# Kernel optimization log

Hardware: AMD Instinct MI355X
Metric: run time of the kernel (lower is better)

Reference implementation:

```python
import jax, jax.numpy as jnp
import numpy as np

P_SIZE = 128   # proto_size
HID = 768      # hidden_size
BATCH = 32
NREL = 16
RATIO = 0.5    # proto_emb_ratio


def setup_inputs() -> dict:
    key = jax.random.key(0)
    k1, k2, k3, k4 = jax.random.split(key, 4)
    return {
        "instance_embedding": jax.random.normal(k1, (BATCH, HID), jnp.float32),
        # small scale keeps sigmoid(p_h @ M_r @ p_t) away from hard saturation
        "relation_embedding": jax.random.normal(k2, (NREL, HID, HID), jnp.float32) * 0.02,
        "rel_label_ids": jax.random.randint(k3, (BATCH, NREL, P_SIZE), 0, P_SIZE + 1, dtype=jnp.int32),
        "labels": jnp.arange(BATCH, dtype=jnp.int32),  # distinct -> torch.unique is exact with static shapes
        "prototypes": jax.random.normal(k4, (P_SIZE, HID), jnp.float32),  # nn.Embedding weight
    }


def reference(instance_embedding, relation_embedding, rel_label_ids, labels, prototypes):
    P, H = prototypes.shape
    B, R, _ = rel_label_ids.shape

    # torch.unique(labels, return_inverse=True): sorted uniques + inverse map.
    labels_unique = jnp.sort(labels)                      # [K] (K == B, labels distinct)
    inv = jnp.argsort(jnp.argsort(labels))                # index_list (rank of each label)
    # original code: index = index_list[k] -> rel rows permuted by inverse map
    rel_k = rel_label_ids[inv]                            # [K,R,P]

    total_nonzero = jnp.sum(rel_label_ids) > 0
    batch_mask = (jnp.sum(rel_k, axis=(1, 2)) > 0)[:, None, None]   # skip if sum(rel[index])==0
    row_mask = (jnp.sum(rel_k, axis=2) > 0)[:, :, None]             # skip if sum(rel[index][i])==0
    m = (rel_k != P) & batch_mask & row_mask & total_nonzero        # [K,R,P] active entries
    mf = m.astype(prototypes.dtype)

    P0 = prototypes                                       # get_proto_embedding(): never updated inside loop
    heads = jnp.minimum(rel_k, P - 1)                     # safe gather (masked where == P)
    Ph = P0[heads]                                        # [K,R,P,H]  (largest intermediate)
    pt = P0[labels_unique]                                # [K,H]

    # sim[k,i,j] = sigmoid(P0[head] @ M_r[i] @ P0[label_k])
    v = jnp.einsum('rhg,kg->krh', relation_embedding, pt)           # [K,R,H]
    sim = jax.nn.sigmoid(jnp.einsum('krph,krh->krp', Ph, v))        # [K,R,P]

    # logits_ol init: zeros, then logits_ol[:][:][:][0] = 1.0 sets the k==0 slab to 1.0
    base = jnp.zeros((B, R, P, 2), prototypes.dtype).at[0].set(1.0)
    l1 = jnp.where(m, sim, base[..., 1])
    l0 = jnp.where(m, 1.0 - sim, base[..., 0])
    logits_ol = jnp.stack([l0, l1], axis=-1).reshape(-1, 2)         # [K*R*P, 2]
    labels_ol = m.astype(jnp.int32).reshape(-1)                     # [K*R*P]

    # proto propagation: mean over active (i,j) of P0[head] @ M_r[i]
    w = jnp.einsum('krp,krph->krh', mf, Ph)                         # [K,R,H]
    prop = jnp.einsum('krh,rhg->kg', w, relation_embedding)         # [K,H]
    n = jnp.sum(mf, axis=(1, 2))                                    # num_prop per k
    prop = prop / jnp.maximum(n, 1.0)[:, None]
    old_rows = prototypes[labels_unique]
    new_rows = RATIO * old_rows + (1.0 - RATIO) * prop
    rows = jnp.where((n > 0)[:, None], new_rows, old_rows)
    proto_embedding = prototypes.at[labels_unique].set(rows)        # scatter update (distinct rows)

    # CrossEntropyLoss (mean); 0 when all rel ids are zero (labels_ol would be None)
    logp = jax.nn.log_softmax(logits_ol, axis=-1)
    ce = -jnp.mean(jnp.take_along_axis(logp, labels_ol[:, None], axis=1))
    loss_ol = jnp.where(total_nonzero, ce, 0.0)

    # logits = -||proto - instance||^2 pairwise: [B, P]
    diff = instance_embedding[:, None, :] - proto_embedding[None, :, :]
    logits = -jnp.sum(diff * diff, axis=2)

    return logits, loss_ol, proto_embedding
```

## Files before the change

kernel.cpp:

```cpp
#include <hip/hip_runtime.h>
#include <hip/hip_bf16.h>
#include <math.h>

#define K_B 32
#define NRELD 16
#define PSZ 128
#define HID 768

using bf16x8 = __attribute__((ext_vector_type(8))) short;
using f32x4  = __attribute__((ext_vector_type(4))) float;

__device__ __forceinline__ unsigned int f2bf(float x) {
    unsigned int u = __float_as_uint(x);
    return (u + 0x7fffu + ((u >> 16) & 1u)) >> 16;
}
__device__ __forceinline__ float bf2f(unsigned short b) {
    return __uint_as_float(((unsigned int)b) << 16);
}

__global__ __launch_bounds__(512) void k_setup(const int* __restrict__ labels,
        const int* __restrict__ rel, int* __restrict__ inv, int* __restrict__ lu,
        int* __restrict__ rowflag, int* __restrict__ batchflag,
        int* __restrict__ total, int* __restrict__ rowOwner,
        float* __restrict__ nAct, float* __restrict__ lossAcc,
        float* __restrict__ prop)
{
    __shared__ int lab[32], rankS[32], luS[32], ownS[128];
    __shared__ int rowflagS[512], cntS[512], bfS[32], totS;
    int t = threadIdx.x;
    if (t < 32) lab[t] = labels[t];
    __syncthreads();
    if (t < 32) {
        int r = 0;
        for (int j = 0; j < 32; ++j) r += (lab[j] < lab[t]);
        rankS[t] = r; inv[t] = r;
    }
    if (t < 128) ownS[t] = -1;
    __syncthreads();
    if (t < 32) luS[rankS[t]] = lab[t];
    __syncthreads();
    if (t < 32) { lu[t] = luS[t]; ownS[luS[t]] = t; }
    __syncthreads();
    if (t < 128) rowOwner[t] = ownS[t];
    {
        int k = t >> 4, i = t & 15;
        const int* rp = rel + ((size_t)rankS[k] * NRELD + i) * PSZ;
        int s = 0, c = 0;
        for (int j = 0; j < PSZ; ++j) { int v_ = rp[j]; s += v_; c += (v_ != PSZ); }
        rowflagS[t] = (s > 0); cntS[t] = c;
        rowflag[t] = (s > 0);
    }
    __syncthreads();
    if (t < 32) {
        int b = 0;
        for (int i = 0; i < 16; ++i) b |= rowflagS[t*16 + i];
        bfS[t] = b; batchflag[t] = b;
    }
    __syncthreads();
    if (t == 0) {
        int tt = 0;
        for (int k = 0; k < 32; ++k) tt |= bfS[k];
        totS = tt; total[0] = tt; lossAcc[0] = 0.f;
    }
    __syncthreads();
    if (t < 32) {
        float n = 0.f;
        if (totS && bfS[t])
            for (int i = 0; i < 16; ++i)
                if (rowflagS[t*16 + i]) n += (float)cntS[t*16 + i];
        nAct[t] = n;
    }
    for (int idx = t; idx < K_B*HID; idx += 512) prop[idx] = 0.f;
}

__global__ __launch_bounds__(192) void k_prep(
        const int* __restrict__ relIds, const int* __restrict__ inv,
        const int* __restrict__ rowflag, const int* __restrict__ batchflag,
        const int* __restrict__ total, const int* __restrict__ rowOwner,
        const float* __restrict__ P0,
        unsigned short* __restrict__ S_bf, unsigned short* __restrict__ P0_bf,
        unsigned short* __restrict__ P0T_bf, unsigned short* __restrict__ pt_bf)
{
    int bid = blockIdx.x, t = threadIdx.x;
    int k = bid >> 4, r = bid & 15;
    __shared__ int hist[128];
    if (t < 128) hist[t] = 0;
    __syncthreads();
    int flag = total[0] && batchflag[k] && rowflag[k*NRELD + r];
    if (flag && t < 128) {
        int id = relIds[((size_t)inv[k]*NRELD + r)*PSZ + t];
        if (id != PSZ) atomicAdd(&hist[id], 1);
    }
    __syncthreads();
    if (t < 128) S_bf[(size_t)bid*128 + t] = (unsigned short)f2bf((float)hist[t]);
    if (bid < 128) {
        int p = bid;
        float4 v4 = *(const float4*)&P0[(size_t)p*HID + t*4];
        unsigned int b0 = f2bf(v4.x), b1 = f2bf(v4.y), b2 = f2bf(v4.z), b3 = f2bf(v4.w);
        uint2 d; d.x = b0 | (b1 << 16); d.y = b2 | (b3 << 16);
        *(uint2*)&P0_bf[(size_t)p*HID + t*4] = d;
        P0T_bf[(size_t)(t*4+0)*128 + p] = (unsigned short)b0;
        P0T_bf[(size_t)(t*4+1)*128 + p] = (unsigned short)b1;
        P0T_bf[(size_t)(t*4+2)*128 + p] = (unsigned short)b2;
        P0T_bf[(size_t)(t*4+3)*128 + p] = (unsigned short)b3;
        int kk = rowOwner[p];
        if (kk >= 0) *(uint2*)&pt_bf[(size_t)kk*HID + t*4] = d;
    }
}

__global__ __launch_bounds__(256) void k_v_mfma(
        const float* __restrict__ rel, const unsigned short* __restrict__ pt_bf,
        unsigned short* __restrict__ v_bf)
{
    int r = blockIdx.x, hs = blockIdx.y, t = threadIdx.x;
    int wave = t >> 6, lane = t & 63;
    __shared__ unsigned short ptS[32*768];
    __shared__ unsigned short AS[64*128];

    for (int i = t; i < 3072; i += 256) {
        int k = i / 96, c = i % 96;
        uint4 d = *(const uint4*)&pt_bf[(size_t)k*HID + c*8];
        *(uint4*)&ptS[k*768 + (c ^ (k & 7))*8] = d;
    }

    const int gq = (t & 31) * 4;
    const int hr = t >> 5;
    const size_t relbase = ((size_t)r*HID + hs*64) * HID;

    float4 buf[8];
    #pragma unroll
    for (int rr = 0; rr < 8; ++rr)
        buf[rr] = *(const float4*)&rel[relbase + (size_t)(hr + rr*8)*HID + gq];

    f32x4 acc[2] = {{0.f,0.f,0.f,0.f},{0.f,0.f,0.f,0.f}};
    const int arow = wave*16 + (lane & 15);

    for (int gt = 0; gt < 6; ++gt) {
        int g0 = gt * 128;
        __syncthreads();
        #pragma unroll
        for (int rr = 0; rr < 8; ++rr) {
            int h_l = hr + rr*8;
            float4 v4 = buf[rr];
            int cs = (gq >> 3) ^ (h_l & 7);
            uint2 d; d.x = f2bf(v4.x) | (f2bf(v4.y) << 16);
            d.y = f2bf(v4.z) | (f2bf(v4.w) << 16);
            *(uint2*)&AS[h_l*128 + cs*8 + (gq & 4)] = d;
        }
        __syncthreads();
        if (gt < 5) {
            int gn = g0 + 128;
            #pragma unroll
            for (int rr = 0; rr < 8; ++rr)
                buf[rr] = *(const float4*)&rel[relbase + (size_t)(hr + rr*8)*HID + gn + gq];
        }
        #pragma unroll
        for (int kk = 0; kk < 4; ++kk) {
            int cA = (kk*4 + (lane >> 4)) ^ (arow & 7);
            bf16x8 a = *(const bf16x8*)&AS[arow*128 + cA*8];
            #pragma unroll
            for (int nf = 0; nf < 2; ++nf) {
                int k = nf*16 + (lane & 15);
                int cB = (gt*16 + kk*4 + (lane >> 4)) ^ (k & 7);
                bf16x8 b = *(const bf16x8*)&ptS[k*768 + cB*8];
                acc[nf] = __builtin_amdgcn_mfma_f32_16x16x32_bf16(a, b, acc[nf], 0, 0, 0);
            }
        }
    }
    int h_out = hs*64 + wave*16 + (lane >> 4) * 4;
    #pragma unroll
    for (int nf = 0; nf < 2; ++nf) {
        int k = nf*16 + (lane & 15);
        uint2 d; d.x = f2bf(acc[nf][0]) | (f2bf(acc[nf][1]) << 16);
        d.y = f2bf(acc[nf][2]) | (f2bf(acc[nf][3]) << 16);
        *(uint2*)&v_bf[((size_t)k*NRELD + r)*HID + h_out] = d;
    }
}

__global__ __launch_bounds__(256) void k_w_mfma(
        const unsigned short* __restrict__ S_bf, const unsigned short* __restrict__ P0T_bf,
        unsigned short* __restrict__ w_bf)
{
    int ms = blockIdx.x, ns = blockIdx.y, t = threadIdx.x;
    int wave = t >> 6, lane = t & 63;
    __shared__ unsigned short AS[64*128], BS2[64*128];
    for (int i = t; i < 1024; i += 256) {
        int row = i >> 4, c = i & 15;
        *(uint4*)&AS[row*128 + (c ^ (row & 7))*8] =
            *(const uint4*)&S_bf[(size_t)(ms*64 + row)*128 + c*8];
        *(uint4*)&BS2[row*128 + (c ^ (row & 7))*8] =
            *(const uint4*)&P0T_bf[(size_t)(ns*64 + row)*128 + c*8];
    }
    __syncthreads();
    f32x4 acc[4] = {{0.f,0.f,0.f,0.f},{0.f,0.f,0.f,0.f},{0.f,0.f,0.f,0.f},{0.f,0.f,0.f,0.f}};
    int arow = wave*16 + (lane & 15);
    #pragma unroll
    for (int kk = 0; kk < 4; ++kk) {
        int cA = (kk*4 + (lane >> 4)) ^ (arow & 7);
        bf16x8 a = *(const bf16x8*)&AS[arow*128 + cA*8];
        #pragma unroll
        for (int nf = 0; nf < 4; ++nf) {
            int brow = nf*16 + (lane & 15);
            int cB = (kk*4 + (lane >> 4)) ^ (brow & 7);
            bf16x8 b = *(const bf16x8*)&BS2[brow*128 + cB*8];
            acc[nf] = __builtin_amdgcn_mfma_f32_16x16x32_bf16(a, b, acc[nf], 0, 0, 0);
        }
    }
    int kr0 = ms*64 + wave*16 + (lane >> 4) * 4;
    #pragma unroll
    for (int nf = 0; nf < 4; ++nf) {
        int h = ns*64 + nf*16 + (lane & 15);
        #pragma unroll
        for (int j = 0; j < 4; ++j)
            w_bf[(size_t)(kr0 + j)*HID + h] = (unsigned short)f2bf(acc[nf][j]);
    }
}

__global__ __launch_bounds__(256) void k_prop_mfma(
        const float* __restrict__ rel, const unsigned short* __restrict__ w_bf,
        float* __restrict__ prop)
{
    int r = blockIdx.x, gs = blockIdx.y, t = threadIdx.x;
    int wave = t >> 6, lane = t & 63;
    __shared__ unsigned short WS[32*768];
    __shared__ unsigned short BS[64*128];

    for (int i = t; i < 3072; i += 256) {
        int k = i / 96, c = i % 96;
        uint4 d = *(const uint4*)&w_bf[((size_t)k*NRELD + r)*HID + c*8];
        *(uint4*)&WS[k*768 + (c ^ (k & 7))*8] = d;
    }

    const int gqq = t & 15;
    const int h4  = t >> 4;
    const size_t relb = (size_t)r*HID*HID + (size_t)gs*64;

    float4 buf[8];
    #pragma unroll
    for (int sup = 0; sup < 2; ++sup)
        #pragma unroll
        for (int rr = 0; rr < 4; ++rr)
            buf[sup*4+rr] = *(const float4*)&rel[relb + (size_t)(sup*64 + h4*4 + rr)*HID + gqq*4];

    f32x4 acc[2] = {{0.f,0.f,0.f,0.f},{0.f,0.f,0.f,0.f}};

    for (int ht = 0; ht < 6; ++ht) {
        int ht0 = ht * 128;
        __syncthreads();
        #pragma unroll
        for (int sup = 0; sup < 2; ++sup) {
            #pragma unroll
            for (int i = 0; i < 4; ++i) {
                int g_l = gqq*4 + i;
                int hloc = sup*64 + h4*4;
                unsigned int p0 = f2bf(((const float*)&buf[sup*4+0])[i]);
                unsigned int p1 = f2bf(((const float*)&buf[sup*4+1])[i]);
                unsigned int p2 = f2bf(((const float*)&buf[sup*4+2])[i]);
                unsigned int p3 = f2bf(((const float*)&buf[sup*4+3])[i]);
                int cs = (hloc >> 3) ^ ((g_l >> 2) & 7);
                uint2 d; d.x = p0 | (p1 << 16); d.y = p2 | (p3 << 16);
                *(uint2*)&BS[g_l*128 + cs*8 + (hloc & 4)] = d;
            }
        }
        __syncthreads();
        if (ht < 5) {
            int hn = ht0 + 128;
            #pragma unroll
            for (int sup = 0; sup < 2; ++sup)
                #pragma unroll
                for (int rr = 0; rr < 4; ++rr)
                    buf[sup*4+rr] = *(const float4*)&rel[relb + (size_t)(hn + sup*64 + h4*4 + rr)*HID + gqq*4];
        }
        int g_l = wave*16 + (lane & 15);
        #pragma unroll
        for (int kk = 0; kk < 4; ++kk) {
            int cB = (kk*4 + (lane >> 4)) ^ ((g_l >> 2) & 7);
            bf16x8 b = *(const bf16x8*)&BS[g_l*128 + cB*8];
            #pragma unroll
            for (int mf = 0; mf < 2; ++mf) {
                int arow = mf*16 + (lane & 15);
                int cA = (ht*16 + kk*4 + (lane >> 4)) ^ (arow & 7);
                bf16x8 a = *(const bf16x8*)&WS[arow*768 + cA*8];
                acc[mf] = __builtin_amdgcn_mfma_f32_16x16x32_bf16(a, b, acc[mf], 0, 0, 0);
            }
        }
    }
    int gcol = gs*64 + wave*16 + (lane & 15);
    #pragma unroll
    for (int mf = 0; mf < 2; ++mf) {
        int k0 = mf*16 + (lane >> 4) * 4;
        #pragma unroll
        for (int j = 0; j < 4; ++j)
            atomicAdd(&prop[(size_t)(k0 + j)*HID + gcol], acc[mf][j]);
    }
}

__global__ __launch_bounds__(256) void k_zzloss(
        const unsigned short* __restrict__ v_bf, const unsigned short* __restrict__ P0_bf,
        const unsigned short* __restrict__ S_bf, float* __restrict__ lossAcc)
{
    int ms = blockIdx.x, t = threadIdx.x;
    int wave = t >> 6, lane = t & 63;
    __shared__ unsigned short AS[16*128], BS2[128*128];
    __shared__ float red[256];
    f32x4 acc[2] = {{0.f,0.f,0.f,0.f},{0.f,0.f,0.f,0.f}};

    for (int ht = 0; ht < 6; ++ht) {
        int h0 = ht * 128;
        __syncthreads();
        {
            int row = t >> 4, c = t & 15;
            *(uint4*)&AS[row*128 + (c ^ (row & 7))*8] =
                *(const uint4*)&v_bf[(size_t)(ms*16 + row)*HID + h0 + c*8];
            #pragma unroll
            for (int q = 0; q < 8; ++q) {
                int j2 = t + q*256;
                int prow = j2 >> 4, c2 = j2 & 15;
                *(uint4*)&BS2[prow*128 + (c2 ^ (prow & 7))*8] =
                    *(const uint4*)&P0_bf[(size_t)prow*HID + h0 + c2*8];
            }
        }
        __syncthreads();
        int arow = lane & 15;
        #pragma unroll
        for (int kk = 0; kk < 4; ++kk) {
            int cA = (kk*4 + (lane >> 4)) ^ (arow & 7);
            bf16x8 a = *(const bf16x8*)&AS[arow*128 + cA*8];
            #pragma unroll
            for (int nf = 0; nf < 2; ++nf) {
                int brow = wave*32 + nf*16 + (lane & 15);
                int cB = (kk*4 + (lane >> 4)) ^ (brow & 7);
                bf16x8 b = *(const bf16x8*)&BS2[brow*128 + cB*8];
                acc[nf] = __builtin_amdgcn_mfma_f32_16x16x32_bf16(a, b, acc[nf], 0, 0, 0);
            }
        }
    }
    float term = 0.f;
    #pragma unroll
    for (int nf = 0; nf < 2; ++nf) {
        int p = wave*32 + nf*16 + (lane & 15);
        int kr0 = ms*16 + (lane >> 4) * 4;
        #pragma unroll
        for (int j = 0; j < 4; ++j) {
            float S = bf2f(S_bf[(size_t)(kr0 + j)*128 + p]);
            if (S != 0.f) {
                float z = acc[nf][j];
                float s = 1.f / (1.f + expf(-z));
                term += S * (logf(expf(1.f - s) + expf(s)) - s);
            }
        }
    }
    red[t] = term;
    __syncthreads();
    for (int off = 128; off; off >>= 1) {
        if (t < off) red[t] += red[t + off];
        __syncthreads();
    }
    if (t == 0) atomicAdd(lossAcc, red[0]);
}

__global__ __launch_bounds__(192) void k_proto(const float* __restrict__ P0,
        const float* __restrict__ prop, const float* __restrict__ nAct,
        const int* __restrict__ rowOwner, float* __restrict__ protoOut)
{
    int p = blockIdx.x, t = threadIdx.x;
    float4 old = *(const float4*)&P0[(size_t)p*HID + t*4];
    float4 o = old;
    int k = rowOwner[p];
    if (k >= 0) {
        float n = nAct[k];
        if (n > 0.f) {
            float4 pr = *(const float4*)&prop[(size_t)k*HID + t*4];
            float invn = 1.f/n;
            o.x = 0.5f*old.x + 0.5f*pr.x*invn;
            o.y = 0.5f*old.y + 0.5f*pr.y*invn;
            o.z = 0.5f*old.z + 0.5f*pr.z*invn;
            o.w = 0.5f*old.w + 0.5f*pr.w*invn;
        }
    }
    *(float4*)&protoOut[(size_t)p*HID + t*4] = o;
}

__global__ __launch_bounds__(128) void k_logits(const float* __restrict__ inst,
        const float* __restrict__ protoOut, const float* __restrict__ lossAcc,
        const int* __restrict__ total, const float* __restrict__ nAct,
        float* __restrict__ outLogits, float* __restrict__ outLoss)
{
    int b = blockIdx.x, t = threadIdx.x;
    __shared__ float iS[768];
    for (int q = 0; q < 6; ++q) iS[t + 128*q] = inst[(size_t)b*HID + t + 128*q];
    __syncthreads();
    const float4* pr = (const float4*)&protoOut[(size_t)t*HID];
    float acc = 0.f;
    for (int q = 0; q < HID/4; ++q) {
        float4 pv = pr[q];
        float dx = iS[q*4+0] - pv.x, dy = iS[q*4+1] - pv.y;
        float dz = iS[q*4+2] - pv.z, dw = iS[q*4+3] - pv.w;
        acc += dx*dx + dy*dy + dz*dz + dw*dw;
    }
    outLogits[b*PSZ + t] = -acc;
    if (b == 0 && t == 0) {
        float na = 0.f;
        for (int k = 0; k < 32; ++k) na += nAct[k];
        outLoss[0] = total[0]
            ? (lossAcc[0] + (65536.f - na) * 0.6931471805599453f) * (1.f/65536.f)
            : 0.f;
    }
}

extern "C" void kernel_launch(void* const* d_in, const int* in_sizes, int n_in,
                              void* d_out, int out_size, void* d_ws, size_t ws_size,
                              hipStream_t stream)
{
    const float* inst  = (const float*)d_in[0];
    const float* rel   = (const float*)d_in[1];
    const int* relIds  = (const int*)d_in[2];
    const int* labels  = (const int*)d_in[3];
    const float* P0    = (const float*)d_in[4];
    float* out = (float*)d_out;
    float* outLogits = out;
    float* outLoss   = out + 4096;
    float* outProto  = out + 4097;

    char* ws = (char*)d_ws;
    unsigned short* v_bf    = (unsigned short*)(ws + 0);
    unsigned short* w_bf    = (unsigned short*)(ws + 786432);
    unsigned short* S_bf    = (unsigned short*)(ws + 1572864);
    unsigned short* P0_bf   = (unsigned short*)(ws + 1703936);
    unsigned short* P0T_bf  = (unsigned short*)(ws + 1900544);
    unsigned short* pt_bf   = (unsigned short*)(ws + 2097152);
    float* prop    = (float*)(ws + 2146304);
    float* nAct    = (float*)(ws + 2244608);
    float* lossAcc = (float*)(ws + 2244736);
    int*   inv     = (int*)(ws + 2244864);
    int*   lu      = (int*)(ws + 2244992);
    int*   rowflag = (int*)(ws + 2245120);
    int*   batchflag = (int*)(ws + 2247168);
    int*   total   = (int*)(ws + 2247296);
    int*   rowOwner= (int*)(ws + 2247424);

    k_setup<<<1, 512, 0, stream>>>(labels, relIds, inv, lu, rowflag, batchflag,
                                   total, rowOwner, nAct, lossAcc, prop);
    k_prep<<<512, 192, 0, stream>>>(relIds, inv, rowflag, batchflag, total,
                                    rowOwner, P0, S_bf, P0_bf, P0T_bf, pt_bf);
    k_v_mfma<<<dim3(16,12), 256, 0, stream>>>(rel, pt_bf, v_bf);
    k_w_mfma<<<dim3(8,12), 256, 0, stream>>>(S_bf, P0T_bf, w_bf);
    k_prop_mfma<<<dim3(16,12), 256, 0, stream>>>(rel, w_bf, prop);
    k_zzloss<<<32, 256, 0, stream>>>(v_bf, P0_bf, S_bf, lossAcc);
    k_proto<<<128, 192, 0, stream>>>(P0, prop, nAct, rowOwner, outProto);
    k_logits<<<32, 128, 0, stream>>>(inst, outProto, lossAcc, total, nAct,
                                     outLogits, outLoss);
}
```

Baseline: 150.7 us.

## Fuse setup into prep, merge v/w GEMMs and loss/proto kernels

Drops the single-block setup kernel. Each prep block now recomputes label ranks and owners in shared memory and derives its own row flag and active count with a block reduction. The v and w MFMA kernels are merged into one 288-block launch that also zeroes prop and the loss accumulator. The loss and proto-update kernels are merged into one launch, with the proto blocks rebuilding per-row active counts from the per-row flags. The aim is to cut launch count from eight to five and remove the serial single-block setup stage, at the cost of redundant rank computation in every prep block and uneven work across blocks in the merged kernels.

```diff
diff --git a/kernel.cpp b/kernel.cpp
--- a/kernel.cpp
+++ b/kernel.cpp
@@ -18,81 +18,48 @@
     return __uint_as_float(((unsigned int)b) << 16);
 }
 
-__global__ __launch_bounds__(512) void k_setup(const int* __restrict__ labels,
-        const int* __restrict__ rel, int* __restrict__ inv, int* __restrict__ lu,
-        int* __restrict__ rowflag, int* __restrict__ batchflag,
-        int* __restrict__ total, int* __restrict__ rowOwner,
-        float* __restrict__ nAct, float* __restrict__ lossAcc,
-        float* __restrict__ prop)
-{
-    __shared__ int lab[32], rankS[32], luS[32], ownS[128];
-    __shared__ int rowflagS[512], cntS[512], bfS[32], totS;
-    int t = threadIdx.x;
-    if (t < 32) lab[t] = labels[t];
-    __syncthreads();
-    if (t < 32) {
-        int r = 0;
-        for (int j = 0; j < 32; ++j) r += (lab[j] < lab[t]);
-        rankS[t] = r; inv[t] = r;
-    }
-    if (t < 128) ownS[t] = -1;
-    __syncthreads();
-    if (t < 32) luS[rankS[t]] = lab[t];
-    __syncthreads();
-    if (t < 32) { lu[t] = luS[t]; ownS[luS[t]] = t; }
-    __syncthreads();
-    if (t < 128) rowOwner[t] = ownS[t];
-    {
-        int k = t >> 4, i = t & 15;
-        const int* rp = rel + ((size_t)rankS[k] * NRELD + i) * PSZ;
-        int s = 0, c = 0;
-        for (int j = 0; j < PSZ; ++j) { int v_ = rp[j]; s += v_; c += (v_ != PSZ); }
-        rowflagS[t] = (s > 0); cntS[t] = c;
-        rowflag[t] = (s > 0);
-    }
-    __syncthreads();
-    if (t < 32) {
-        int b = 0;
-        for (int i = 0; i < 16; ++i) b |= rowflagS[t*16 + i];
-        bfS[t] = b; batchflag[t] = b;
-    }
-    __syncthreads();
-    if (t == 0) {
-        int tt = 0;
-        for (int k = 0; k < 32; ++k) tt |= bfS[k];
-        totS = tt; total[0] = tt; lossAcc[0] = 0.f;
-    }
-    __syncthreads();
-    if (t < 32) {
-        float n = 0.f;
-        if (totS && bfS[t])
-            for (int i = 0; i < 16; ++i)
-                if (rowflagS[t*16 + i]) n += (float)cntS[t*16 + i];
-        nAct[t] = n;
-    }
-    for (int idx = t; idx < K_B*HID; idx += 512) prop[idx] = 0.f;
-}
-
 __global__ __launch_bounds__(192) void k_prep(
-        const int* __restrict__ relIds, const int* __restrict__ inv,
-        const int* __restrict__ rowflag, const int* __restrict__ batchflag,
-        const int* __restrict__ total, const int* __restrict__ rowOwner,
+        const int* __restrict__ labels, const int* __restrict__ relIds,
         const float* __restrict__ P0,
         unsigned short* __restrict__ S_bf, unsigned short* __restrict__ P0_bf,
-        unsigned short* __restrict__ P0T_bf, unsigned short* __restrict__ pt_bf)
+        unsigned short* __restrict__ P0T_bf, unsigned short* __restrict__ pt_bf,
+        int* __restrict__ rowflag, int* __restrict__ cntRow,
+        int* __restrict__ rowOwner_g)
 {
     int bid = blockIdx.x, t = threadIdx.x;
     int k = bid >> 4, r = bid & 15;
-    __shared__ int hist[128];
-    if (t < 128) hist[t] = 0;
-    __syncthreads();
-    int flag = total[0] && batchflag[k] && rowflag[k*NRELD + r];
-    if (flag && t < 128) {
-        int id = relIds[((size_t)inv[k]*NRELD + r)*PSZ + t];
-        if (id != PSZ) atomicAdd(&hist[id], 1);
-    }
-    __syncthreads();
-    if (t < 128) S_bf[(size_t)bid*128 + t] = (unsigned short)f2bf((float)hist[t]);
+    __shared__ int lab[32], rankS[32], luS[32], ownS[128];
+    __shared__ int hist[128], redS[128];
+    if (t < 32) lab[t] = labels[t];
+    if (t < 128) { hist[t] = 0; ownS[t] = -1; }
+    __syncthreads();
+    if (t < 32) { int rk = 0; for (int j = 0; j < 32; ++j) rk += (lab[j] < lab[t]); rankS[t] = rk; }
+    __syncthreads();
+    if (t < 32) luS[rankS[t]] = lab[t];
+    __syncthreads();
+    if (t < 32) ownS[luS[t]] = t;
+    __syncthreads();
+
+    int id = 0, isv = 0;
+    if (t < 128) {
+        id = relIds[((size_t)rankS[k]*NRELD + r)*PSZ + t];
+        isv = (id != PSZ);
+        if (isv) atomicAdd(&hist[id], 1);
+        redS[t] = id + (isv << 20);
+    }
+    __syncthreads();
+    for (int off = 64; off; off >>= 1) {
+        if (t < off) redS[t] += redS[t + off];
+        __syncthreads();
+    }
+    int rowsum = redS[0] & 0xFFFFF;
+    int cnt    = redS[0] >> 20;
+    int rf     = (rowsum > 0);
+    if (t < 128)
+        S_bf[(size_t)bid*128 + t] = (unsigned short)f2bf(rf ? (float)hist[t] : 0.f);
+    if (t == 0) { rowflag[bid] = rf; cntRow[bid] = cnt; }
+    if (bid == 0 && t < 128) rowOwner_g[t] = ownS[t];
+
     if (bid < 128) {
         int p = bid;
         float4 v4 = *(const float4*)&P0[(size_t)p*HID + t*4];
@@ -103,116 +70,120 @@
         P0T_bf[(size_t)(t*4+1)*128 + p] = (unsigned short)b1;
         P0T_bf[(size_t)(t*4+2)*128 + p] = (unsigned short)b2;
         P0T_bf[(size_t)(t*4+3)*128 + p] = (unsigned short)b3;
-        int kk = rowOwner[p];
+        int kk = ownS[p];
         if (kk >= 0) *(uint2*)&pt_bf[(size_t)kk*HID + t*4] = d;
     }
 }
 
-__global__ __launch_bounds__(256) void k_v_mfma(
+__global__ __launch_bounds__(256) void k_vw(
         const float* __restrict__ rel, const unsigned short* __restrict__ pt_bf,
-        unsigned short* __restrict__ v_bf)
-{
-    int r = blockIdx.x, hs = blockIdx.y, t = threadIdx.x;
+        const unsigned short* __restrict__ S_bf, const unsigned short* __restrict__ P0T_bf,
+        unsigned short* __restrict__ v_bf, unsigned short* __restrict__ w_bf,
+        float* __restrict__ prop, float* __restrict__ lossAcc)
+{
+    __shared__ unsigned short sh[32*768 + 64*128];
+    int bid = blockIdx.x, t = threadIdx.x;
     int wave = t >> 6, lane = t & 63;
-    __shared__ unsigned short ptS[32*768];
-    __shared__ unsigned short AS[64*128];
-
-    for (int i = t; i < 3072; i += 256) {
-        int k = i / 96, c = i % 96;
-        uint4 d = *(const uint4*)&pt_bf[(size_t)k*HID + c*8];
-        *(uint4*)&ptS[k*768 + (c ^ (k & 7))*8] = d;
-    }
-
-    const int gq = (t & 31) * 4;
-    const int hr = t >> 5;
-    const size_t relbase = ((size_t)r*HID + hs*64) * HID;
-
-    float4 buf[8];
-    #pragma unroll
-    for (int rr = 0; rr < 8; ++rr)
-        buf[rr] = *(const float4*)&rel[relbase + (size_t)(hr + rr*8)*HID + gq];
-
-    f32x4 acc[2] = {{0.f,0.f,0.f,0.f},{0.f,0.f,0.f,0.f}};
-    const int arow = wave*16 + (lane & 15);
-
-    for (int gt = 0; gt < 6; ++gt) {
-        int g0 = gt * 128;
-        __syncthreads();
-        #pragma unroll
-        for (int rr = 0; rr < 8; ++rr) {
-            int h_l = hr + rr*8;
-            float4 v4 = buf[rr];
-            int cs = (gq >> 3) ^ (h_l & 7);
-            uint2 d; d.x = f2bf(v4.x) | (f2bf(v4.y) << 16);
-            d.y = f2bf(v4.z) | (f2bf(v4.w) << 16);
-            *(uint2*)&AS[h_l*128 + cs*8 + (gq & 4)] = d;
-        }
-        __syncthreads();
-        if (gt < 5) {
-            int gn = g0 + 128;
-            #pragma unroll
-            for (int rr = 0; rr < 8; ++rr)
-                buf[rr] = *(const float4*)&rel[relbase + (size_t)(hr + rr*8)*HID + gn + gq];
-        }
+
+    if (bid < 192) {
+        int r = bid & 15, hs = bid >> 4;
+        unsigned short* ptS = sh;
+        unsigned short* AS  = sh + 32*768;
+
+        for (int i = t; i < 3072; i += 256) {
+            int k = i / 96, c = i % 96;
+            uint4 d = *(const uint4*)&pt_bf[(size_t)k*HID + c*8];
+            *(uint4*)&ptS[k*768 + (c ^ (k & 7))*8] = d;
+        }
+        const int gq = (t & 31) * 4;
+        const int hr = t >> 5;
+        const size_t relbase = ((size_t)r*HID + hs*64) * HID;
+
+        float4 buf[8];
+        #pragma unroll
+        for (int rr = 0; rr < 8; ++rr)
+            buf[rr] = *(const float4*)&rel[relbase + (size_t)(hr + rr*8)*HID + gq];
+
+        f32x4 acc[2] = {{0.f,0.f,0.f,0.f},{0.f,0.f,0.f,0.f}};
+        const int arow = wave*16 + (lane & 15);
+
+        for (int gt = 0; gt < 6; ++gt) {
+            __syncthreads();
+            #pragma unroll
+            for (int rr = 0; rr < 8; ++rr) {
+                int h_l = hr + rr*8;
+                float4 v4 = buf[rr];
+                int cs = (gq >> 3) ^ (h_l & 7);
+                uint2 d; d.x = f2bf(v4.x) | (f2bf(v4.y) << 16);
+                d.y = f2bf(v4.z) | (f2bf(v4.w) << 16);
+                *(uint2*)&AS[h_l*128 + cs*8 + (gq & 4)] = d;
+            }
+            __syncthreads();
+            if (gt < 5) {
+                int gn = gt*128 + 128;
+                #pragma unroll
+                for (int rr = 0; rr < 8; ++rr)
+                    buf[rr] = *(const float4*)&rel[relbase + (size_t)(hr + rr*8)*HID + gn + gq];
+            }
+            #pragma unroll
+            for (int kk = 0; kk < 4; ++kk) {
+                int cA = (kk*4 + (lane >> 4)) ^ (arow & 7);
+                bf16x8 a = *(const bf16x8*)&AS[arow*128 + cA*8];
+                #pragma unroll
+                for (int nf = 0; nf < 2; ++nf) {
+                    int k = nf*16 + (lane & 15);
+                    int cB = (gt*16 + kk*4 + (lane >> 4)) ^ (k & 7);
+                    bf16x8 b = *(const bf16x8*)&ptS[k*768 + cB*8];
+                    acc[nf] = __builtin_amdgcn_mfma_f32_16x16x32_bf16(a, b, acc[nf], 0, 0, 0);
+                }
+            }
+        }
+        int h_out = hs*64 + wave*16 + (lane >> 4) * 4;
+        #pragma unroll
+        for (int nf = 0; nf < 2; ++nf) {
+            int k = nf*16 + (lane & 15);
+            uint2 d; d.x = f2bf(acc[nf][0]) | (f2bf(acc[nf][1]) << 16);
+            d.y = f2bf(acc[nf][2]) | (f2bf(acc[nf][3]) << 16);
+            *(uint2*)&v_bf[((size_t)k*NRELD + r)*HID + h_out] = d;
+        }
+    } else {
+        int idx = bid - 192;
+        int ms = idx / 12, ns = idx % 12;
+        unsigned short* AS2 = sh;
+        unsigned short* BS2 = sh + 64*128;
+        if (t < 64) *(float4*)&prop[idx*256 + t*4] = float4{0.f,0.f,0.f,0.f};
+        if (idx == 0 && t == 0) lossAcc[0] = 0.f;
+
+        for (int i = t; i < 1024; i += 256) {
+            int row = i >> 4, c = i & 15;
+            *(uint4*)&AS2[row*128 + (c ^ (row & 7))*8] =
+                *(const uint4*)&S_bf[(size_t)(ms*64 + row)*128 + c*8];
+            *(uint4*)&BS2[row*128 + (c ^ (row & 7))*8] =
+                *(const uint4*)&P0T_bf[(size_t)(ns*64 + row)*128 + c*8];
+        }
+        __syncthreads();
+        f32x4 acc[4] = {{0.f,0.f,0.f,0.f},{0.f,0.f,0.f,0.f},{0.f,0.f,0.f,0.f},{0.f,0.f,0.f,0.f}};
+        int arow = wave*16 + (lane & 15);
         #pragma unroll
         for (int kk = 0; kk < 4; ++kk) {
             int cA = (kk*4 + (lane >> 4)) ^ (arow & 7);
-            bf16x8 a = *(const bf16x8*)&AS[arow*128 + cA*8];
-            #pragma unroll
-            for (int nf = 0; nf < 2; ++nf) {
-                int k = nf*16 + (lane & 15);
-                int cB = (gt*16 + kk*4 + (lane >> 4)) ^ (k & 7);
-                bf16x8 b = *(const bf16x8*)&ptS[k*768 + cB*8];
+            bf16x8 a = *(const bf16x8*)&AS2[arow*128 + cA*8];
+            #pragma unroll
+            for (int nf = 0; nf < 4; ++nf) {
+                int brow = nf*16 + (lane & 15);
+                int cB = (kk*4 + (lane >> 4)) ^ (brow & 7);
+                bf16x8 b = *(const bf16x8*)&BS2[brow*128 + cB*8];
                 acc[nf] = __builtin_amdgcn_mfma_f32_16x16x32_bf16(a, b, acc[nf], 0, 0, 0);
             }
         }
-    }
-    int h_out = hs*64 + wave*16 + (lane >> 4) * 4;
-    #pragma unroll
-    for (int nf = 0; nf < 2; ++nf) {
-        int k = nf*16 + (lane & 15);
-        uint2 d; d.x = f2bf(acc[nf][0]) | (f2bf(acc[nf][1]) << 16);
-        d.y = f2bf(acc[nf][2]) | (f2bf(acc[nf][3]) << 16);
-        *(uint2*)&v_bf[((size_t)k*NRELD + r)*HID + h_out] = d;
-    }
-}
-
-__global__ __launch_bounds__(256) void k_w_mfma(
-        const unsigned short* __restrict__ S_bf, const unsigned short* __restrict__ P0T_bf,
-        unsigned short* __restrict__ w_bf)
-{
-    int ms = blockIdx.x, ns = blockIdx.y, t = threadIdx.x;
-    int wave = t >> 6, lane = t & 63;
-    __shared__ unsigned short AS[64*128], BS2[64*128];
-    for (int i = t; i < 1024; i += 256) {
-        int row = i >> 4, c = i & 15;
-        *(uint4*)&AS[row*128 + (c ^ (row & 7))*8] =
-            *(const uint4*)&S_bf[(size_t)(ms*64 + row)*128 + c*8];
-        *(uint4*)&BS2[row*128 + (c ^ (row & 7))*8] =
-            *(const uint4*)&P0T_bf[(size_t)(ns*64 + row)*128 + c*8];
-    }
-    __syncthreads();
-    f32x4 acc[4] = {{0.f,0.f,0.f,0.f},{0.f,0.f,0.f,0.f},{0.f,0.f,0.f,0.f},{0.f,0.f,0.f,0.f}};
-    int arow = wave*16 + (lane & 15);
-    #pragma unroll
-    for (int kk = 0; kk < 4; ++kk) {
-        int cA = (kk*4 + (lane >> 4)) ^ (arow & 7);
-        bf16x8 a = *(const bf16x8*)&AS[arow*128 + cA*8];
+        int kr0 = ms*64 + wave*16 + (lane >> 4) * 4;
         #pragma unroll
         for (int nf = 0; nf < 4; ++nf) {
-            int brow = nf*16 + (lane & 15);
-            int cB = (kk*4 + (lane >> 4)) ^ (brow & 7);
-            bf16x8 b = *(const bf16x8*)&BS2[brow*128 + cB*8];
-            acc[nf] = __builtin_amdgcn_mfma_f32_16x16x32_bf16(a, b, acc[nf], 0, 0, 0);
-        }
-    }
-    int kr0 = ms*64 + wave*16 + (lane >> 4) * 4;
-    #pragma unroll
-    for (int nf = 0; nf < 4; ++nf) {
-        int h = ns*64 + nf*16 + (lane & 15);
-        #pragma unroll
-        for (int j = 0; j < 4; ++j)
-            w_bf[(size_t)(kr0 + j)*HID + h] = (unsigned short)f2bf(acc[nf][j]);
+            int h = ns*64 + nf*16 + (lane & 15);
+            #pragma unroll
+            for (int j = 0; j < 4; ++j)
+                w_bf[(size_t)(kr0 + j)*HID + h] = (unsigned short)f2bf(acc[nf][j]);
+        }
     }
 }
 
@@ -230,7 +201,6 @@
         uint4 d = *(const uint4*)&w_bf[((size_t)k*NRELD + r)*HID + c*8];
         *(uint4*)&WS[k*768 + (c ^ (k & 7))*8] = d;
     }
-
     const int gqq = t & 15;
     const int h4  = t >> 4;
     const size_t relb = (size_t)r*HID*HID + (size_t)gs*64;
@@ -245,7 +215,6 @@
     f32x4 acc[2] = {{0.f,0.f,0.f,0.f},{0.f,0.f,0.f,0.f}};
 
     for (int ht = 0; ht < 6; ++ht) {
-        int ht0 = ht * 128;
         __syncthreads();
         #pragma unroll
         for (int sup = 0; sup < 2; ++sup) {
@@ -264,7 +233,7 @@
         }
         __syncthreads();
         if (ht < 5) {
-            int hn = ht0 + 128;
+            int hn = ht*128 + 128;
             #pragma unroll
             for (int sup = 0; sup < 2; ++sup)
                 #pragma unroll
@@ -295,99 +264,120 @@
     }
 }
 
-__global__ __launch_bounds__(256) void k_zzloss(
+__global__ __launch_bounds__(256) void k_zzproto(
         const unsigned short* __restrict__ v_bf, const unsigned short* __restrict__ P0_bf,
-        const unsigned short* __restrict__ S_bf, float* __restrict__ lossAcc)
-{
-    int ms = blockIdx.x, t = threadIdx.x;
+        const unsigned short* __restrict__ S_bf, float* __restrict__ lossAcc,
+        const float* __restrict__ P0, const float* __restrict__ prop,
+        const int* __restrict__ rowflag, const int* __restrict__ cntRow,
+        const int* __restrict__ rowOwner_g, float* __restrict__ protoOut)
+{
+    __shared__ unsigned short sh[16*128 + 128*128];
+    __shared__ float red[256];
+    __shared__ float nActS[32];
+    __shared__ int kS[32];
+    int bid = blockIdx.x, t = threadIdx.x;
     int wave = t >> 6, lane = t & 63;
-    __shared__ unsigned short AS[16*128], BS2[128*128];
-    __shared__ float red[256];
-    f32x4 acc[2] = {{0.f,0.f,0.f,0.f},{0.f,0.f,0.f,0.f}};
-
-    for (int ht = 0; ht < 6; ++ht) {
-        int h0 = ht * 128;
-        __syncthreads();
-        {
-            int row = t >> 4, c = t & 15;
-            *(uint4*)&AS[row*128 + (c ^ (row & 7))*8] =
-                *(const uint4*)&v_bf[(size_t)(ms*16 + row)*HID + h0 + c*8];
-            #pragma unroll
-            for (int q = 0; q < 8; ++q) {
-                int j2 = t + q*256;
-                int prow = j2 >> 4, c2 = j2 & 15;
-                *(uint4*)&BS2[prow*128 + (c2 ^ (prow & 7))*8] =
-                    *(const uint4*)&P0_bf[(size_t)prow*HID + h0 + c2*8];
-            }
-        }
-        __syncthreads();
-        int arow = lane & 15;
-        #pragma unroll
-        for (int kk = 0; kk < 4; ++kk) {
-            int cA = (kk*4 + (lane >> 4)) ^ (arow & 7);
-            bf16x8 a = *(const bf16x8*)&AS[arow*128 + cA*8];
-            #pragma unroll
-            for (int nf = 0; nf < 2; ++nf) {
-                int brow = wave*32 + nf*16 + (lane & 15);
-                int cB = (kk*4 + (lane >> 4)) ^ (brow & 7);
-                bf16x8 b = *(const bf16x8*)&BS2[brow*128 + cB*8];
-                acc[nf] = __builtin_amdgcn_mfma_f32_16x16x32_bf16(a, b, acc[nf], 0, 0, 0);
-            }
-        }
-    }
-    float term = 0.f;
-    #pragma unroll
-    for (int nf = 0; nf < 2; ++nf) {
-        int p = wave*32 + nf*16 + (lane & 15);
-        int kr0 = ms*16 + (lane >> 4) * 4;
-        #pragma unroll
-        for (int j = 0; j < 4; ++j) {
-            float S = bf2f(S_bf[(size_t)(kr0 + j)*128 + p]);
-            if (S != 0.f) {
-                float z = acc[nf][j];
-                float s = 1.f / (1.f + expf(-z));
-                term += S * (logf(expf(1.f - s) + expf(s)) - s);
-            }
-        }
-    }
-    red[t] = term;
-    __syncthreads();
-    for (int off = 128; off; off >>= 1) {
-        if (t < off) red[t] += red[t + off];
-        __syncthreads();
-    }
-    if (t == 0) atomicAdd(lossAcc, red[0]);
-}
-
-__global__ __launch_bounds__(192) void k_proto(const float* __restrict__ P0,
-        const float* __restrict__ prop, const float* __restrict__ nAct,
-        const int* __restrict__ rowOwner, float* __restrict__ protoOut)
-{
-    int p = blockIdx.x, t = threadIdx.x;
-    float4 old = *(const float4*)&P0[(size_t)p*HID + t*4];
-    float4 o = old;
-    int k = rowOwner[p];
-    if (k >= 0) {
-        float n = nAct[k];
-        if (n > 0.f) {
-            float4 pr = *(const float4*)&prop[(size_t)k*HID + t*4];
-            float invn = 1.f/n;
-            o.x = 0.5f*old.x + 0.5f*pr.x*invn;
-            o.y = 0.5f*old.y + 0.5f*pr.y*invn;
-            o.z = 0.5f*old.z + 0.5f*pr.z*invn;
-            o.w = 0.5f*old.w + 0.5f*pr.w*invn;
-        }
-    }
-    *(float4*)&protoOut[(size_t)p*HID + t*4] = o;
+
+    if (bid < 32) {
+        int ms = bid;
+        unsigned short* AS  = sh;
+        unsigned short* BS2 = sh + 16*128;
+        f32x4 acc[2] = {{0.f,0.f,0.f,0.f},{0.f,0.f,0.f,0.f}};
+        for (int ht = 0; ht < 6; ++ht) {
+            int h0 = ht * 128;
+            __syncthreads();
+            {
+                int row = t >> 4, c = t & 15;
+                *(uint4*)&AS[row*128 + (c ^ (row & 7))*8] =
+                    *(const uint4*)&v_bf[(size_t)(ms*16 + row)*HID + h0 + c*8];
+                #pragma unroll
+                for (int q = 0; q < 8; ++q) {
+                    int j2 = t + q*256;
+                    int prow = j2 >> 4, c2 = j2 & 15;
+                    *(uint4*)&BS2[prow*128 + (c2 ^ (prow & 7))*8] =
+                        *(const uint4*)&P0_bf[(size_t)prow*HID + h0 + c2*8];
+                }
+            }
+            __syncthreads();
+            int arow = lane & 15;
+            #pragma unroll
+            for (int kk = 0; kk < 4; ++kk) {
+                int cA = (kk*4 + (lane >> 4)) ^ (arow & 7);
+                bf16x8 a = *(const bf16x8*)&AS[arow*128 + cA*8];
+                #pragma unroll
+                for (int nf = 0; nf < 2; ++nf) {
+                    int brow = wave*32 + nf*16 + (lane & 15);
+                    int cB = (kk*4 + (lane >> 4)) ^ (brow & 7);
+                    bf16x8 b = *(const bf16x8*)&BS2[brow*128 + cB*8];
+                    acc[nf] = __builtin_amdgcn_mfma_f32_16x16x32_bf16(a, b, acc[nf], 0, 0, 0);
+                }
+            }
+        }
+        float term = 0.f;
+        #pragma unroll
+        for (int nf = 0; nf < 2; ++nf) {
+            int p = wave*32 + nf*16 + (lane & 15);
+            int kr0 = ms*16 + (lane >> 4) * 4;
+            #pragma unroll
+            for (int j = 0; j < 4; ++j) {
+                float S = bf2f(S_bf[(size_t)(kr0 + j)*128 + p]);
+                if (S != 0.f) {
+                    float z = acc[nf][j];
+                    float s = 1.f / (1.f + expf(-z));
+                    term += S * (logf(expf(1.f - s) + expf(s)) - s);
+                }
+            }
+        }
+        red[t] = term;
+        __syncthreads();
+        for (int off = 128; off; off >>= 1) {
+            if (t < off) red[t] += red[t + off];
+            __syncthreads();
+        }
+        if (t == 0) atomicAdd(lossAcc, red[0]);
+    } else {
+        int base = (bid - 32) * 32;
+        if (t < 32) {
+            int p = base + t;
+            int k = rowOwner_g[p];
+            float n = 0.f;
+            if (k >= 0)
+                for (int i = 0; i < 16; ++i) {
+                    int rr = k*NRELD + i;
+                    if (rowflag[rr]) n += (float)cntRow[rr];
+                }
+            nActS[t] = n; kS[t] = k;
+        }
+        __syncthreads();
+        for (int j = 0; j < 24; ++j) {
+            int flat = t + 256*j;
+            int pl = flat / 192, c = flat % 192;
+            int p = base + pl;
+            float4 old = *(const float4*)&P0[(size_t)p*HID + c*4];
+            float4 o = old;
+            int k = kS[pl]; float n = nActS[pl];
+            if (k >= 0 && n > 0.f) {
+                float4 pr = *(const float4*)&prop[(size_t)k*HID + c*4];
+                float invn = 0.5f / n;
+                o.x = 0.5f*old.x + pr.x*invn;
+                o.y = 0.5f*old.y + pr.y*invn;
+                o.z = 0.5f*old.z + pr.z*invn;
+                o.w = 0.5f*old.w + pr.w*invn;
+            }
+            *(float4*)&protoOut[(size_t)p*HID + c*4] = o;
+        }
+    }
 }
 
 __global__ __launch_bounds__(128) void k_logits(const float* __restrict__ inst,
         const float* __restrict__ protoOut, const float* __restrict__ lossAcc,
-        const int* __restrict__ total, const float* __restrict__ nAct,
+        const int* __restrict__ rowflag, const int* __restrict__ cntRow,
         float* __restrict__ outLogits, float* __restrict__ outLoss)
 {
     int b = blockIdx.x, t = threadIdx.x;
     __shared__ float iS[768];
+    __shared__ float ls[128];
+    __shared__ int ts[128];
     for (int q = 0; q < 6; ++q) iS[t + 128*q] = inst[(size_t)b*HID + t + 128*q];
     __syncthreads();
     const float4* pr = (const float4*)&protoOut[(size_t)t*HID];
@@ -399,12 +389,25 @@
         acc += dx*dx + dy*dy + dz*dz + dw*dw;
     }
     outLogits[b*PSZ + t] = -acc;
-    if (b == 0 && t == 0) {
-        float na = 0.f;
-        for (int k = 0; k < 32; ++k) na += nAct[k];
-        outLoss[0] = total[0]
-            ? (lossAcc[0] + (65536.f - na) * 0.6931471805599453f) * (1.f/65536.f)
-            : 0.f;
+    if (b == 0) {
+        float s = 0.f; int tot = 0;
+        #pragma unroll
+        for (int q = 0; q < 4; ++q) {
+            int rr = t + 128*q;
+            int rf = rowflag[rr];
+            tot |= rf;
+            if (rf) s += (float)cntRow[rr];
+        }
+        ls[t] = s; ts[t] = tot;
+        __syncthreads();
+        for (int off = 64; off; off >>= 1) {
+            if (t < off) { ls[t] += ls[t + off]; ts[t] |= ts[t + off]; }
+            __syncthreads();
+        }
+        if (t == 0)
+            outLoss[0] = ts[0]
+                ? (lossAcc[0] + (65536.f - ls[0]) * 0.6931471805599453f) * (1.f/65536.f)
+                : 0.f;
     }
 }
 
@@ -430,24 +433,18 @@
     unsigned short* P0T_bf  = (unsigned short*)(ws + 1900544);
     unsigned short* pt_bf   = (unsigned short*)(ws + 2097152);
     float* prop    = (float*)(ws + 2146304);
-    float* nAct    = (float*)(ws + 2244608);
-    float* lossAcc = (float*)(ws + 2244736);
-    int*   inv     = (int*)(ws + 2244864);
-    int*   lu      = (int*)(ws + 2244992);
-    int*   rowflag = (int*)(ws + 2245120);
-    int*   batchflag = (int*)(ws + 2247168);
-    int*   total   = (int*)(ws + 2247296);
-    int*   rowOwner= (int*)(ws + 2247424);
-
-    k_setup<<<1, 512, 0, stream>>>(labels, relIds, inv, lu, rowflag, batchflag,
-                                   total, rowOwner, nAct, lossAcc, prop);
-    k_prep<<<512, 192, 0, stream>>>(relIds, inv, rowflag, batchflag, total,
-                                    rowOwner, P0, S_bf, P0_bf, P0T_bf, pt_bf);
-    k_v_mfma<<<dim3(16,12), 256, 0, stream>>>(rel, pt_bf, v_bf);
-    k_w_mfma<<<dim3(8,12), 256, 0, stream>>>(S_bf, P0T_bf, w_bf);
+    float* lossAcc = (float*)(ws + 2244608);
+    int*   rowflag = (int*)(ws + 2244736);
+    int*   cntRow  = (int*)(ws + 2246784);
+    int*   rowOwner= (int*)(ws + 2248832);
+
+    k_prep<<<512, 192, 0, stream>>>(labels, relIds, P0, S_bf, P0_bf, P0T_bf,
+                                    pt_bf, rowflag, cntRow, rowOwner);
+    k_vw<<<288, 256, 0, stream>>>(rel, pt_bf, S_bf, P0T_bf, v_bf, w_bf,
+                                  prop, lossAcc);
     k_prop_mfma<<<dim3(16,12), 256, 0, stream>>>(rel, w_bf, prop);
-    k_zzloss<<<32, 256, 0, stream>>>(v_bf, P0_bf, S_bf, lossAcc);
-    k_proto<<<128, 192, 0, stream>>>(P0, prop, nAct, rowOwner, outProto);
-    k_logits<<<32, 128, 0, stream>>>(inst, outProto, lossAcc, total, nAct,
+    k_zzproto<<<36, 256, 0, stream>>>(v_bf, P0_bf, S_bf, lossAcc, P0, prop,
+                                      rowflag, cntRow, rowOwner, outProto);
+    k_logits<<<32, 128, 0, stream>>>(inst, outProto, lossAcc, rowflag, cntRow,
                                      outLogits, outLoss);
 }
```

After: 136.5 us. 9.4% less time.
